# Optimization experiments

Measured on AMD Instinct MI355X. Metric: run time of the kernel, lower is better.

The kernel has to match this reference:

```python
import jax, jax.numpy as jnp
import numpy as np

NUM_EXPERTS = 8
NUM_SPIKE_EXPERTS = 2
TOTAL_EXPERTS = NUM_EXPERTS + NUM_SPIKE_EXPERTS
D_IN = 512
HIDDEN = 1024  # expert_dim == spike_expert_capacity
D_OUT = 256
TOP_K = 2


def setup_inputs() -> dict:
    key = jax.random.key(0)
    ks = jax.random.split(key, 8)
    B, T = 32768, 16
    x = jax.random.normal(ks[0], (B, D_IN), dtype=jnp.float32)
    spike_indicators = jax.random.uniform(ks[1], (B, T), dtype=jnp.float32)
    s = 0.02
    Wr = jax.random.normal(ks[2], (D_IN, TOTAL_EXPERTS), dtype=jnp.float32) * s
    br = jnp.zeros((TOTAL_EXPERTS,), dtype=jnp.float32)
    W1 = jax.random.normal(ks[3], (TOTAL_EXPERTS, D_IN, HIDDEN), dtype=jnp.float32) * s
    b1 = jnp.zeros((TOTAL_EXPERTS, HIDDEN), dtype=jnp.float32)
    W2 = jax.random.normal(ks[4], (TOTAL_EXPERTS, HIDDEN, D_OUT), dtype=jnp.float32) * s
    b2 = jnp.zeros((TOTAL_EXPERTS, D_OUT), dtype=jnp.float32)
    return {"x": x, "spike_indicators": spike_indicators, "Wr": Wr, "br": br,
            "W1": W1, "b1": b1, "W2": W2, "b2": b2}


def reference(x, spike_indicators, Wr, br, W1, b1, W2, b2):
    # Router logits (plain Dense router branch)
    router_logits = x @ Wr + br                                   # [B, E]
    # Spike-expert routing bias: mean spike indicator added to spike experts only
    spike_mask = jnp.concatenate(
        [jnp.zeros((NUM_EXPERTS,), x.dtype), jnp.ones((NUM_SPIKE_EXPERTS,), x.dtype)])
    avg_spike = jnp.mean(spike_indicators, axis=1, keepdims=True)  # [B, 1]
    adjusted = router_logits + avg_spike * spike_mask[None, :]
    router_probs = jax.nn.softmax(adjusted, axis=-1)               # [B, E]
    top_k_probs, top_k_idx = jax.lax.top_k(router_probs, TOP_K)    # [B, K]
    top_k_norm = top_k_probs / (jnp.sum(top_k_probs, axis=1, keepdims=True) + 1e-9)
    # All experts computed for all tokens (matches original dense loop)
    h = jax.nn.relu(jnp.einsum('bd,edh->beh', x, W1) + b1[None])   # [B, E, H]
    expert_stack = jnp.einsum('beh,eho->beo', h, W2) + b2[None]    # [B, E, O]
    # Gather top-k expert outputs per token and combine
    gathered = jnp.take_along_axis(expert_stack, top_k_idx[:, :, None], axis=1)  # [B, K, O]
    mixed = jnp.sum(gathered * top_k_norm[:, :, None], axis=1)     # [B, O]
    return mixed
```

## Files before the change

kernel.cpp:

```cpp
#include <hip/hip_runtime.h>
#include <hip/hip_bf16.h>
#include <stdint.h>
#include <stddef.h>

typedef __attribute__((ext_vector_type(8))) short short8;
typedef __attribute__((ext_vector_type(4))) float f32x4;

#define NTOK 32768
#define DIN 512
#define HID 1024
#define DOUT 256
#define NEXP 10

__device__ __forceinline__ unsigned short f2bf(float f) {
  unsigned int u = __float_as_uint(f);
  u += 0x7fffu + ((u >> 16) & 1u);
  return (unsigned short)(u >> 16);
}

__device__ __forceinline__ void gld16(void* lds, const void* g) {
  __builtin_amdgcn_global_load_lds(
      (const __attribute__((address_space(1))) unsigned int*)g,
      (__attribute__((address_space(3))) unsigned int*)lds, 16, 0, 0);
}

__global__ void k_transpose_wr(const float* __restrict__ wr, float* __restrict__ wrt) {
  for (int i = threadIdx.x; i < DIN * NEXP; i += 256) {
    int d = i / NEXP, e = i % NEXP;
    wrt[e * DIN + d] = wr[i];
  }
}

__global__ __launch_bounds__(256) void k_transpose_conv(
    const float* __restrict__ in, unsigned short* __restrict__ out, int R, int C) {
  __shared__ unsigned short tile[64][72];
  int tid = threadIdx.x;
  const float* ip = in + ((size_t)blockIdx.z * R + blockIdx.y * 64) * C + blockIdx.x * 64;
  int r = tid >> 2, c0 = (tid & 3) * 16;
  const float* p = ip + (size_t)r * C + c0;
#pragma unroll
  for (int j = 0; j < 16; j += 4) {
    float4 v = *(const float4*)(p + j);
    tile[r][c0 + j + 0] = f2bf(v.x);
    tile[r][c0 + j + 1] = f2bf(v.y);
    tile[r][c0 + j + 2] = f2bf(v.z);
    tile[r][c0 + j + 3] = f2bf(v.w);
  }
  __syncthreads();
  unsigned short* op = out + ((size_t)blockIdx.z * C + blockIdx.x * 64) * R + blockIdx.y * 64;
  int c = tid >> 2, r0 = (tid & 3) * 16;
  unsigned short* q = op + (size_t)c * R + r0;
  union { short8 v; unsigned short u[8]; } t0, t1;
#pragma unroll
  for (int j = 0; j < 8; j++) { t0.u[j] = tile[r0 + j][c]; t1.u[j] = tile[r0 + 8 + j][c]; }
  *(short8*)(q) = t0.v;
  *(short8*)(q + 8) = t1.v;
}

__global__ __launch_bounds__(256) void k_router(
    const float* __restrict__ x, const float* __restrict__ spike,
    const float* __restrict__ wrt, const float* __restrict__ br,
    unsigned short* __restrict__ xb, int* __restrict__ cnt,
    int* __restrict__ tok, float* __restrict__ wgt) {
  __shared__ int s_i0[64], s_i1[64];
  __shared__ float s_w0[64], s_w1[64];
  __shared__ int hist[NEXP], base_[NEXP], loc[NEXP];
  int tid = threadIdx.x, wave = tid >> 6, lane = tid & 63;
  if (tid < NEXP) { hist[tid] = 0; loc[tid] = 0; }
  __syncthreads();
  for (int t = 0; t < 16; t++) {
    int slot = wave * 16 + t;
    int b = blockIdx.x * 64 + slot;
    const float* xr = x + (size_t)b * DIN;
    float xv[8];
#pragma unroll
    for (int k = 0; k < 8; k++) xv[k] = xr[lane + 64 * k];
    unsigned short* xo = xb + (size_t)b * DIN;
#pragma unroll
    for (int k = 0; k < 8; k++) xo[lane + 64 * k] = f2bf(xv[k]);
    float lg[NEXP];
#pragma unroll
    for (int e = 0; e < NEXP; e++) {
      const float* w = wrt + e * DIN;
      float s = 0.f;
#pragma unroll
      for (int k = 0; k < 8; k++) s += xv[k] * w[lane + 64 * k];
      lg[e] = s;
    }
#pragma unroll
    for (int off = 32; off > 0; off >>= 1) {
#pragma unroll
      for (int e = 0; e < NEXP; e++) lg[e] += __shfl_xor(lg[e], off);
    }
    float sv = spike[(size_t)b * 16 + (lane & 15)];
    sv += __shfl_xor(sv, 8); sv += __shfl_xor(sv, 4);
    sv += __shfl_xor(sv, 2); sv += __shfl_xor(sv, 1);
    float avg = sv * 0.0625f;
#pragma unroll
    for (int e = 0; e < NEXP; e++) lg[e] += br[e];
    lg[8] += avg; lg[9] += avg;
    float mx = lg[0];
#pragma unroll
    for (int e = 1; e < NEXP; e++) mx = fmaxf(mx, lg[e]);
    float p[NEXP], ps = 0.f;
#pragma unroll
    for (int e = 0; e < NEXP; e++) { p[e] = __expf(lg[e] - mx); ps += p[e]; }
    int i0 = 0; float p0 = p[0];
#pragma unroll
    for (int e = 1; e < NEXP; e++) if (p[e] > p0) { p0 = p[e]; i0 = e; }
    float p1 = -1.f; int i1 = 0;
#pragma unroll
    for (int e = 0; e < NEXP; e++) if (e != i0 && p[e] > p1) { p1 = p[e]; i1 = e; }
    float inv = 1.f / (p0 + p1 + ps * 1e-9f);
    if (lane == 0) {
      s_i0[slot] = i0; s_i1[slot] = i1;
      s_w0[slot] = p0 * inv; s_w1[slot] = p1 * inv;
      atomicAdd(&hist[i0], 1); atomicAdd(&hist[i1], 1);
    }
  }
  __syncthreads();
  if (tid < NEXP) base_[tid] = atomicAdd(&cnt[tid], hist[tid]);
  __syncthreads();
  if (tid < 64) {
    int b = blockIdx.x * 64 + tid;
    int i0 = s_i0[tid], i1 = s_i1[tid];
    int s0 = base_[i0] + atomicAdd(&loc[i0], 1);
    tok[i0 * NTOK + s0] = b; wgt[i0 * NTOK + s0] = s_w0[tid];
    int s1 = base_[i1] + atomicAdd(&loc[i1], 1);
    tok[i1 * NTOK + s1] = b; wgt[i1 * NTOK + s1] = s_w1[tid];
  }
}

__global__ __launch_bounds__(512, 2) void k_moe(
    const unsigned short* __restrict__ xb, const unsigned short* __restrict__ w1t,
    const unsigned short* __restrict__ w2t, const float* __restrict__ b1,
    const float* __restrict__ b2, const int* __restrict__ cnt,
    const int* __restrict__ tok, const float* __restrict__ wgt,
    float* __restrict__ out) {
  int e = blockIdx.y;
  int n = cnt[e];
  int tile = blockIdx.x;
  if (tile * 128 >= n) return;
  __shared__ unsigned short xa[2][8192];
  __shared__ unsigned short b1h[2][8192];
  __shared__ unsigned short b2h[2][8192];
  __shared__ unsigned short hsh[16384];
  __shared__ int stok[128];
  __shared__ float swgt[128];
  int tid = threadIdx.x;
  if (tid < 128) {
    int idx = tile * 128 + tid;
    bool v = idx < n;
    stok[tid] = v ? tok[e * NTOK + idx] : 0;
    swgt[tid] = v ? wgt[e * NTOK + idx] : 0.f;
  }
  __syncthreads();
  int wave = tid >> 6, lane = tid & 63, quad = lane >> 4, l16 = lane & 15;
  int wm = wave & 1, wn = wave >> 1;
  int srow = tid >> 3;
  int sc8 = (tid & 7) ^ (srow & 7);
  const unsigned short* w1e = w1t + (size_t)e * HID * DIN;
  const unsigned short* w2e = w2t + (size_t)e * DOUT * HID;
  const unsigned short* gxA = xb + (size_t)stok[srow] * DIN + sc8 * 8;
  const unsigned short* gxB = xb + (size_t)stok[64 + srow] * DIN + sc8 * 8;
  const unsigned short* g1A = w1e + (size_t)srow * DIN + sc8 * 8;
  const unsigned short* g2A = w2e + (size_t)(2 * srow + (sc8 >> 2)) * HID + (sc8 & 3) * 8;

#define STAGE_X(nb, ks) do { \
    gld16(&xa[nb][(unsigned)tid * 8], gxA + (ks) * 64); \
    gld16(&xa[nb][((unsigned)tid + 512) * 8], gxB + (ks) * 64); } while (0)
#define STAGE_W1(nb, hcv, ks) do { \
    const unsigned short* p_ = g1A + (size_t)(hcv) * 128 * DIN + (ks) * 64; \
    gld16(&b1h[nb][(unsigned)tid * 8], p_); \
    gld16(&b1h[nb][((unsigned)tid + 512) * 8], p_ + 64 * DIN); } while (0)
#define STAGE_W2(nb, hcv, k2) do { \
    const unsigned short* p_ = g2A + (hcv) * 128 + (k2) * 32; \
    gld16(&b2h[nb][(unsigned)tid * 8], p_); \
    gld16(&b2h[nb][((unsigned)tid + 512) * 8], p_ + 128 * HID); } while (0)

  f32x4 acc2[4][4];
#pragma unroll
  for (int nt = 0; nt < 4; nt++) {
    float bv = b2[e * DOUT + wn * 64 + nt * 16 + l16];
    acc2[0][nt] = (f32x4){bv, bv, bv, bv};
    acc2[1][nt] = (f32x4){bv, bv, bv, bv};
    acc2[2][nt] = (f32x4){bv, bv, bv, bv};
    acc2[3][nt] = (f32x4){bv, bv, bv, bv};
  }
  STAGE_X(0, 0);
  STAGE_W1(0, 0, 0);
  __syncthreads();

  for (int hc = 0; hc < 8; hc++) {
    float bb0 = b1[e * HID + hc * 128 + wn * 32 + l16];
    float bb1v = b1[e * HID + hc * 128 + wn * 32 + 16 + l16];
    f32x4 acc1[4][2];
#pragma unroll
    for (int mt = 0; mt < 4; mt++) {
      acc1[mt][0] = (f32x4){0.f, 0.f, 0.f, 0.f};
      acc1[mt][1] = (f32x4){0.f, 0.f, 0.f, 0.f};
    }
#pragma unroll
    for (int ks = 0; ks < 8; ks++) {
      if (ks < 7) {
        STAGE_X((ks + 1) & 1, ks + 1);
        STAGE_W1((ks + 1) & 1, hc, ks + 1);
      } else {
        int hcn = hc < 7 ? hc + 1 : 7;
        STAGE_X(0, 0);
        STAGE_W1(0, hcn, 0);
      }
      if (ks == 0) STAGE_W2(0, hc, 0);
      if (ks == 1) STAGE_W2(1, hc, 1);
      const unsigned short* xab = xa[ks & 1];
      const unsigned short* w1b = b1h[ks & 1];
#pragma unroll
      for (int ki2 = 0; ki2 < 2; ki2++) {
        int cq = ki2 * 4 + quad;
        short8 af[4], bf[2];
#pragma unroll
        for (int mt = 0; mt < 4; mt++) {
          int r = wm * 64 + mt * 16 + l16;
          af[mt] = *(const short8*)(xab + ((unsigned)(r * 8 + (cq ^ (r & 7)))) * 8);
        }
#pragma unroll
        for (int nt = 0; nt < 2; nt++) {
          int r = wn * 32 + nt * 16 + l16;
          bf[nt] = *(const short8*)(w1b + ((unsigned)(r * 8 + (cq ^ (r & 7)))) * 8);
        }
#pragma unroll
        for (int mt = 0; mt < 4; mt++)
#pragma unroll
          for (int nt = 0; nt < 2; nt++)
            acc1[mt][nt] = __builtin_amdgcn_mfma_f32_16x16x32_bf16(
                af[mt], bf[nt], acc1[mt][nt], 0, 0, 0);
      }
      __syncthreads();
    }
#pragma unroll
    for (int mt = 0; mt < 4; mt++) {
#pragma unroll
      for (int nt = 0; nt < 2; nt++) {
        int col = wn * 32 + nt * 16 + l16;
        int c16 = col >> 3, co = col & 7;
        float bb = nt ? bb1v : bb0;
#pragma unroll
        for (int r4 = 0; r4 < 4; r4++) {
          int r = wm * 64 + mt * 16 + quad * 4 + r4;
          float v = acc1[mt][nt][r4] + bb;
          hsh[((unsigned)(r * 16 + (c16 ^ (r & 15)))) * 8 + co] = f2bf(v > 0.f ? v : 0.f);
        }
      }
    }
    __syncthreads();
#pragma unroll
    for (int k2 = 0; k2 < 4; k2++) {
      if (k2 == 1) STAGE_W2(0, hc, 2);
      if (k2 == 2) STAGE_W2(1, hc, 3);
      const unsigned short* b2b = b2h[k2 & 1];
      short8 af[4], bf[4];
      int c16 = k2 * 4 + quad;
#pragma unroll
      for (int mt = 0; mt < 4; mt++) {
        int r = wm * 64 + mt * 16 + l16;
        af[mt] = *(const short8*)(&hsh[((unsigned)(r * 16 + (c16 ^ (r & 15)))) * 8]);
      }
#pragma unroll
      for (int nt = 0; nt < 4; nt++) {
        int r = wn * 64 + nt * 16 + l16;
        int inner = (((r & 1) << 2) | quad) ^ ((r >> 1) & 7);
        bf[nt] = *(const short8*)(&b2b[((unsigned)((r >> 1) * 8 + inner)) * 8]);
      }
#pragma unroll
      for (int mt = 0; mt < 4; mt++)
#pragma unroll
        for (int nt = 0; nt < 4; nt++)
          acc2[mt][nt] = __builtin_amdgcn_mfma_f32_16x16x32_bf16(
              af[mt], bf[nt], acc2[mt][nt], 0, 0, 0);
      __syncthreads();
    }
  }
#pragma unroll
  for (int mt = 0; mt < 4; mt++) {
#pragma unroll
    for (int r4 = 0; r4 < 4; r4++) {
      int m = wm * 64 + mt * 16 + quad * 4 + r4;
      float wv = swgt[m];
      if (wv != 0.f) {
        int t = stok[m];
        float* op = out + (size_t)t * DOUT + wn * 64 + l16;
#pragma unroll
        for (int nt = 0; nt < 4; nt++)
          atomicAdd(op + nt * 16, acc2[mt][nt][r4] * wv);
      }
    }
  }
#undef STAGE_X
#undef STAGE_W1
#undef STAGE_W2
}

extern "C" void kernel_launch(void* const* d_in, const int* in_sizes, int n_in,
                              void* d_out, int out_size, void* d_ws, size_t ws_size,
                              hipStream_t stream) {
  (void)in_sizes; (void)n_in; (void)ws_size;
  const float* x     = (const float*)d_in[0];
  const float* spike = (const float*)d_in[1];
  const float* Wr    = (const float*)d_in[2];
  const float* br    = (const float*)d_in[3];
  const float* W1    = (const float*)d_in[4];
  const float* b1    = (const float*)d_in[5];
  const float* W2    = (const float*)d_in[6];
  const float* b2    = (const float*)d_in[7];
  float* out = (float*)d_out;
  char* ws = (char*)d_ws;
  unsigned short* xb  = (unsigned short*)(ws + 0);
  unsigned short* w1t = (unsigned short*)(ws + 33554432);
  unsigned short* w2t = (unsigned short*)(ws + 44040192);
  float* wrt          = (float*)(ws + 49283072);
  int*   cnt          = (int*)(ws + 49303552);
  int*   tok          = (int*)(ws + 49303616);
  float* wgt          = (float*)(ws + 50614336);

  hipMemsetAsync(cnt, 0, 64, stream);
  hipMemsetAsync(out, 0, (size_t)out_size * sizeof(float), stream);
  k_transpose_wr<<<1, 256, 0, stream>>>(Wr, wrt);
  k_transpose_conv<<<dim3(16, 8, 10), 256, 0, stream>>>(W1, w1t, DIN, HID);
  k_transpose_conv<<<dim3(4, 16, 10), 256, 0, stream>>>(W2, w2t, HID, DOUT);
  k_router<<<512, 256, 0, stream>>>(x, spike, wrt, br, xb, cnt, tok, wgt);
  k_moe<<<dim3(256, NEXP), 512, 0, stream>>>(xb, w1t, w2t, b1, b2, cnt, tok, wgt, out);
}
```

Measured before the change: 447.4 us.

## Triple-buffer MoE kernel pipeline with explicit vmcnt waits and halved hidden chunks

Restructures the fused MoE kernel to use a three-stage LDS ring buffer. Loads are issued two steps ahead and waited on with explicit s_waitcnt vmcnt plus raw barriers instead of __syncthreads. The hidden chunk drops from 128 to 64 columns, run as 16 iterations, so LDS fits the extra buffers, and b1 bias values are preloaded into registers. MFMA sections are wrapped in s_setprio, and the tiny Wr transpose now runs on 20 blocks instead of one. The aim is to hide global-load latency better, at the cost of more outer iterations and fragile hand-counted wait depths.

```diff
diff --git a/kernel.cpp b/kernel.cpp
--- a/kernel.cpp
+++ b/kernel.cpp
@@ -24,8 +24,10 @@
       (__attribute__((address_space(3))) unsigned int*)lds, 16, 0, 0);
 }
 
-__global__ void k_transpose_wr(const float* __restrict__ wr, float* __restrict__ wrt) {
-  for (int i = threadIdx.x; i < DIN * NEXP; i += 256) {
+__global__ __launch_bounds__(256) void k_transpose_wr(
+    const float* __restrict__ wr, float* __restrict__ wrt) {
+  int i = blockIdx.x * 256 + threadIdx.x;
+  if (i < DIN * NEXP) {
     int d = i / NEXP, e = i % NEXP;
     wrt[e * DIN + d] = wr[i];
   }
@@ -141,10 +143,10 @@
   int n = cnt[e];
   int tile = blockIdx.x;
   if (tile * 128 >= n) return;
-  __shared__ unsigned short xa[2][8192];
-  __shared__ unsigned short b1h[2][8192];
-  __shared__ unsigned short b2h[2][8192];
-  __shared__ unsigned short hsh[16384];
+  __shared__ unsigned short xa[3][8192];
+  __shared__ unsigned short w1s[3][4096];
+  __shared__ unsigned short w2s[3][8192];
+  __shared__ unsigned short hs[8192];
   __shared__ int stok[128];
   __shared__ float swgt[128];
   int tid = threadIdx.x;
@@ -166,18 +168,9 @@
   const unsigned short* g1A = w1e + (size_t)srow * DIN + sc8 * 8;
   const unsigned short* g2A = w2e + (size_t)(2 * srow + (sc8 >> 2)) * HID + (sc8 & 3) * 8;
 
-#define STAGE_X(nb, ks) do { \
-    gld16(&xa[nb][(unsigned)tid * 8], gxA + (ks) * 64); \
-    gld16(&xa[nb][((unsigned)tid + 512) * 8], gxB + (ks) * 64); } while (0)
-#define STAGE_W1(nb, hcv, ks) do { \
-    const unsigned short* p_ = g1A + (size_t)(hcv) * 128 * DIN + (ks) * 64; \
-    gld16(&b1h[nb][(unsigned)tid * 8], p_); \
-    gld16(&b1h[nb][((unsigned)tid + 512) * 8], p_ + 64 * DIN); } while (0)
-#define STAGE_W2(nb, hcv, k2) do { \
-    const unsigned short* p_ = g2A + (hcv) * 128 + (k2) * 32; \
-    gld16(&b2h[nb][(unsigned)tid * 8], p_); \
-    gld16(&b2h[nb][((unsigned)tid + 512) * 8], p_ + 128 * HID); } while (0)
-
+  float bb[16];
+#pragma unroll
+  for (int h = 0; h < 16; h++) bb[h] = b1[e * HID + h * 64 + wn * 16 + l16];
   f32x4 acc2[4][4];
 #pragma unroll
   for (int nt = 0; nt < 4; nt++) {
@@ -187,83 +180,86 @@
     acc2[2][nt] = (f32x4){bv, bv, bv, bv};
     acc2[3][nt] = (f32x4){bv, bv, bv, bv};
   }
-  STAGE_X(0, 0);
-  STAGE_W1(0, 0, 0);
-  __syncthreads();
-
-  for (int hc = 0; hc < 8; hc++) {
-    float bb0 = b1[e * HID + hc * 128 + wn * 32 + l16];
-    float bb1v = b1[e * HID + hc * 128 + wn * 32 + 16 + l16];
-    f32x4 acc1[4][2];
-#pragma unroll
-    for (int mt = 0; mt < 4; mt++) {
-      acc1[mt][0] = (f32x4){0.f, 0.f, 0.f, 0.f};
-      acc1[mt][1] = (f32x4){0.f, 0.f, 0.f, 0.f};
-    }
+
+#define ISS_G(buf, hcv, ks) do { \
+    gld16(&xa[buf][(unsigned)tid * 8], gxA + (ks) * 64); \
+    gld16(&xa[buf][((unsigned)tid + 512) * 8], gxB + (ks) * 64); \
+    gld16(&w1s[buf][(unsigned)tid * 8], g1A + (size_t)(hcv) * 64 * DIN + (ks) * 64); \
+  } while (0)
+#define ISS_V(buf, hcv, j) do { \
+    const unsigned short* p_ = g2A + (hcv) * 64 + (j) * 32; \
+    gld16(&w2s[buf][(unsigned)tid * 8], p_); \
+    gld16(&w2s[buf][((unsigned)tid + 512) * 8], p_ + 128 * HID); \
+  } while (0)
+#define PWAIT(N) do { \
+    asm volatile("s_waitcnt vmcnt(" #N ") lgkmcnt(0)" ::: "memory"); \
+    __builtin_amdgcn_s_barrier(); \
+    __builtin_amdgcn_sched_barrier(0); \
+  } while (0)
+
+  ISS_G(0, 0, 0);
+  ISS_G(1, 0, 1);
+
+  for (int hc = 0; hc < 16; hc++) {
+    int g0 = (hc * 8) % 3;
+    int v0 = (hc * 2) % 3;
+    int hcn = hc < 15 ? hc + 1 : 15;
+    f32x4 acc1[4];
+#pragma unroll
+    for (int mt = 0; mt < 4; mt++) acc1[mt] = (f32x4){0.f, 0.f, 0.f, 0.f};
 #pragma unroll
     for (int ks = 0; ks < 8; ks++) {
-      if (ks < 7) {
-        STAGE_X((ks + 1) & 1, ks + 1);
-        STAGE_W1((ks + 1) & 1, hc, ks + 1);
-      } else {
-        int hcn = hc < 7 ? hc + 1 : 7;
-        STAGE_X(0, 0);
-        STAGE_W1(0, hcn, 0);
-      }
-      if (ks == 0) STAGE_W2(0, hc, 0);
-      if (ks == 1) STAGE_W2(1, hc, 1);
-      const unsigned short* xab = xa[ks & 1];
-      const unsigned short* w1b = b1h[ks & 1];
+      if (ks < 7) { PWAIT(3); } else { PWAIT(2); }
+      if (ks < 6)       ISS_G((g0 + ks + 2) % 3, hc, ks + 2);
+      else if (ks == 6) ISS_V(v0, hc, 0);
+      else              ISS_V((v0 + 1) % 3, hc, 1);
+      const unsigned short* xab = xa[(g0 + ks) % 3];
+      const unsigned short* w1b = w1s[(g0 + ks) % 3];
+      __builtin_amdgcn_s_setprio(1);
 #pragma unroll
       for (int ki2 = 0; ki2 < 2; ki2++) {
         int cq = ki2 * 4 + quad;
-        short8 af[4], bf[2];
+        short8 af[4], bfr;
 #pragma unroll
         for (int mt = 0; mt < 4; mt++) {
           int r = wm * 64 + mt * 16 + l16;
           af[mt] = *(const short8*)(xab + ((unsigned)(r * 8 + (cq ^ (r & 7)))) * 8);
         }
-#pragma unroll
-        for (int nt = 0; nt < 2; nt++) {
-          int r = wn * 32 + nt * 16 + l16;
-          bf[nt] = *(const short8*)(w1b + ((unsigned)(r * 8 + (cq ^ (r & 7)))) * 8);
+        {
+          int r = wn * 16 + l16;
+          bfr = *(const short8*)(w1b + ((unsigned)(r * 8 + (cq ^ (r & 7)))) * 8);
         }
 #pragma unroll
         for (int mt = 0; mt < 4; mt++)
-#pragma unroll
-          for (int nt = 0; nt < 2; nt++)
-            acc1[mt][nt] = __builtin_amdgcn_mfma_f32_16x16x32_bf16(
-                af[mt], bf[nt], acc1[mt][nt], 0, 0, 0);
-      }
-      __syncthreads();
-    }
-#pragma unroll
-    for (int mt = 0; mt < 4; mt++) {
-#pragma unroll
-      for (int nt = 0; nt < 2; nt++) {
-        int col = wn * 32 + nt * 16 + l16;
+          acc1[mt] = __builtin_amdgcn_mfma_f32_16x16x32_bf16(af[mt], bfr, acc1[mt], 0, 0, 0);
+      }
+      __builtin_amdgcn_s_setprio(0);
+      if (ks == 7) {
+        float bbv = bb[hc];
+        int col = wn * 16 + l16;
         int c16 = col >> 3, co = col & 7;
-        float bb = nt ? bb1v : bb0;
-#pragma unroll
-        for (int r4 = 0; r4 < 4; r4++) {
-          int r = wm * 64 + mt * 16 + quad * 4 + r4;
-          float v = acc1[mt][nt][r4] + bb;
-          hsh[((unsigned)(r * 16 + (c16 ^ (r & 15)))) * 8 + co] = f2bf(v > 0.f ? v : 0.f);
+#pragma unroll
+        for (int mt = 0; mt < 4; mt++) {
+#pragma unroll
+          for (int r4 = 0; r4 < 4; r4++) {
+            int r = wm * 64 + mt * 16 + quad * 4 + r4;
+            float v = acc1[mt][r4] + bbv;
+            hs[((unsigned)(r * 8 + (c16 ^ (r & 7)))) * 8 + co] = f2bf(v > 0.f ? v : 0.f);
+          }
         }
       }
     }
-    __syncthreads();
-#pragma unroll
-    for (int k2 = 0; k2 < 4; k2++) {
-      if (k2 == 1) STAGE_W2(0, hc, 2);
-      if (k2 == 2) STAGE_W2(1, hc, 3);
-      const unsigned short* b2b = b2h[k2 & 1];
+#pragma unroll
+    for (int j = 0; j < 2; j++) {
+      if (j == 0) { PWAIT(2); ISS_G((g0 + 2) % 3, hcn, 0); }
+      else        { PWAIT(3); ISS_G(g0, hcn, 1); }
+      const unsigned short* b2b = w2s[j == 0 ? v0 : (v0 + 1) % 3];
       short8 af[4], bf[4];
-      int c16 = k2 * 4 + quad;
+      int c16 = j * 4 + quad;
 #pragma unroll
       for (int mt = 0; mt < 4; mt++) {
         int r = wm * 64 + mt * 16 + l16;
-        af[mt] = *(const short8*)(&hsh[((unsigned)(r * 16 + (c16 ^ (r & 15)))) * 8]);
+        af[mt] = *(const short8*)(&hs[((unsigned)(r * 8 + (c16 ^ (r & 7)))) * 8]);
       }
 #pragma unroll
       for (int nt = 0; nt < 4; nt++) {
@@ -271,13 +267,14 @@
         int inner = (((r & 1) << 2) | quad) ^ ((r >> 1) & 7);
         bf[nt] = *(const short8*)(&b2b[((unsigned)((r >> 1) * 8 + inner)) * 8]);
       }
+      __builtin_amdgcn_s_setprio(1);
 #pragma unroll
       for (int mt = 0; mt < 4; mt++)
 #pragma unroll
         for (int nt = 0; nt < 4; nt++)
           acc2[mt][nt] = __builtin_amdgcn_mfma_f32_16x16x32_bf16(
               af[mt], bf[nt], acc2[mt][nt], 0, 0, 0);
-      __syncthreads();
+      __builtin_amdgcn_s_setprio(0);
     }
   }
 #pragma unroll
@@ -295,9 +292,9 @@
       }
     }
   }
-#undef STAGE_X
-#undef STAGE_W1
-#undef STAGE_W2
+#undef ISS_G
+#undef ISS_V
+#undef PWAIT
 }
 
 extern "C" void kernel_launch(void* const* d_in, const int* in_sizes, int n_in,
@@ -324,7 +321,7 @@
 
   hipMemsetAsync(cnt, 0, 64, stream);
   hipMemsetAsync(out, 0, (size_t)out_size * sizeof(float), stream);
-  k_transpose_wr<<<1, 256, 0, stream>>>(Wr, wrt);
+  k_transpose_wr<<<20, 256, 0, stream>>>(Wr, wrt);
   k_transpose_conv<<<dim3(16, 8, 10), 256, 0, stream>>>(W1, w1t, DIN, HID);
   k_transpose_conv<<<dim3(4, 16, 10), 256, 0, stream>>>(W2, w2t, HID, DOUT);
   k_router<<<512, 256, 0, stream>>>(x, spike, wrt, br, xb, cnt, tok, wgt);
```

Measured after the change: 503.5 us. +12.5%, slower.
